# Kernel optimization log

Hardware: AMD Instinct MI355X
Metric: run time of the kernel (lower is better)

The kernel has to match this reference:

```python
import jax, jax.numpy as jnp
import numpy as np

L, D = 8192, 1024


def binary_operator_diag(q_i, q_j):
    # elementwise (diagonal) linear-recurrence combine: h_j = A_j * h_i + b_j
    A_i, b_i = q_i
    A_j, b_j = q_j
    return A_j * A_i, A_j * b_i + b_j


def setup_inputs() -> dict:
    key = jax.random.key(0)
    k_in, k_u, k_th, k_bre, k_bim = jax.random.split(key, 5)
    inputs = jax.random.normal(k_in, (L, D), dtype=jnp.float32)
    # stable LRU init: |lambda| = exp(-exp(nu)) = sqrt(u), u in (0.01, 0.99)
    u = jax.random.uniform(k_u, (D,), jnp.float32, 0.01, 0.99)
    nu = jnp.log(-0.5 * jnp.log(u))
    # phase stored in log-space (forward uses exp(theta))
    theta = jnp.log(jax.random.uniform(k_th, (D,), jnp.float32, 1e-3, 6.28))
    gamma_log = 0.5 * jnp.log(1.0 - u)  # = log(sqrt(1 - |lambda|^2))
    norm = np.float32(np.sqrt(2.0 * D))
    B_re = jax.random.normal(k_bre, (D, D), jnp.float32) / norm
    B_im = jax.random.normal(k_bim, (D, D), jnp.float32) / norm
    return {"inputs": inputs, "theta": theta, "nu": nu,
            "gamma_log": gamma_log, "B_re": B_re, "B_im": B_im}


def reference(inputs, theta, nu, gamma_log, B_re, B_im):
    # diagonal transition: lambda = exp(-exp(nu) + i*exp(theta)), shape [D]
    diag_lambda = jnp.exp(-jnp.exp(nu) + 1j * jnp.exp(theta))
    # normalized input matrix: (B_re + i B_im) * exp(gamma_log)[:, None]
    B_norm = (B_re + 1j * B_im) * jnp.exp(gamma_log)[:, None]  # [D, D] complex
    # Bu[t] = B_norm @ u_t  -> batched as one GEMM: [L, D] complex
    Bu = jnp.einsum('ld,kd->lk', inputs.astype(B_norm.dtype), B_norm)
    Lambda_elements = jnp.broadcast_to(diag_lambda[None, :], Bu.shape)
    # parallel associative scan over time (axis 0), elementwise over channels
    _, hidden_states = jax.lax.associative_scan(
        binary_operator_diag, (Lambda_elements, Bu))
    return hidden_states.real + inputs
```

## Files before the change

### kernel.cpp

```cpp
#include <hip/hip_runtime.h>
#include <cstdint>
#include <cstddef>

typedef float  f32x4   __attribute__((ext_vector_type(4)));
typedef short  bf16x8  __attribute__((ext_vector_type(8)));
typedef unsigned short u16x8 __attribute__((ext_vector_type(8)));

#define L_SEQ   8192
#define D_DIM   1024
#define N_COL   2048
#define N_PAIR  512
#define CHUNK_T 16
#define N_CHUNK 512

__device__ __forceinline__ unsigned short f2bf(float f) {
  unsigned int b = __float_as_uint(f);
  b += 0x7FFFu + ((b >> 16) & 1u);
  return (unsigned short)(b >> 16);
}
__device__ __forceinline__ float bf2f(unsigned short u) {
  return __uint_as_float((unsigned int)u << 16);
}
__device__ __forceinline__ void gload_lds16(const void* g, void* lds) {
  __builtin_amdgcn_global_load_lds(
      (const __attribute__((address_space(1))) void*)g,
      (__attribute__((address_space(3))) void*)lds, 16, 0, 0);
}
__device__ __forceinline__ float2 cmul(float2 a, float2 b) {
  return make_float2(a.x * b.x - a.y * b.y, a.x * b.y + a.y * b.x);
}
__device__ __forceinline__ float2 csqr(float2 a) {
  return make_float2(a.x * a.x - a.y * a.y, 2.f * a.x * a.y);
}
__device__ __forceinline__ void cfma2(const float4& lm, float2& h0, float2& h1,
                                      const float4& v) {
  float nr0 = fmaf(lm.x, h0.x, fmaf(-lm.y, h0.y, v.x));
  float ni0 = fmaf(lm.x, h0.y, fmaf(lm.y, h0.x, v.y));
  float nr1 = fmaf(lm.z, h1.x, fmaf(-lm.w, h1.y, v.z));
  float ni1 = fmaf(lm.z, h1.y, fmaf(lm.w, h1.x, v.w));
  h0.x = nr0; h0.y = ni0; h1.x = nr1; h1.y = ni1;
}

__global__ __launch_bounds__(256) void k_prep(
    const float* __restrict__ in, const float* __restrict__ Bre,
    const float* __restrict__ Bim, const float* __restrict__ gamma_log,
    const float* __restrict__ theta, const float* __restrict__ nu,
    unsigned short* __restrict__ A, unsigned short* __restrict__ W,
    float2* __restrict__ lam) {
  int b = blockIdx.x;
  if (b < 4096) {
    int i = b * 256 + threadIdx.x;
    const float4* p = (const float4*)in;
    float4 a = p[2 * i], c = p[2 * i + 1];
    u16x8 o;
    o[0] = f2bf(a.x); o[1] = f2bf(a.y); o[2] = f2bf(a.z); o[3] = f2bf(a.w);
    o[4] = f2bf(c.x); o[5] = f2bf(c.y); o[6] = f2bf(c.z); o[7] = f2bf(c.w);
    *(u16x8*)(A + (size_t)i * 8) = o;
  } else if (b < 5120) {
    int t = (b - 4096) * 256 + threadIdx.x;
    int row = t >> 7;
    int seg = t & 127;
    int k = row >> 1;
    const float* src = (row & 1) ? Bim : Bre;
    float g = expf(gamma_log[k]);
    const float4* p = (const float4*)(src + (size_t)k * D_DIM + seg * 8);
    float4 a = p[0], c = p[1];
    u16x8 o;
    o[0] = f2bf(a.x * g); o[1] = f2bf(a.y * g); o[2] = f2bf(a.z * g); o[3] = f2bf(a.w * g);
    o[4] = f2bf(c.x * g); o[5] = f2bf(c.y * g); o[6] = f2bf(c.z * g); o[7] = f2bf(c.w * g);
    *(u16x8*)(W + (size_t)row * D_DIM + seg * 8) = o;
  } else {
    int k = (b - 5120) * 256 + threadIdx.x;
    if (k < D_DIM) {
      float mod = expf(-expf(nu[k]));
      float ang = expf(theta[k]);
      lam[k] = make_float2(mod * cosf(ang), mod * sinf(ang));
    }
  }
}

__global__ __launch_bounds__(256, 2) void k_gemm(const unsigned short* __restrict__ A,
                                                 const unsigned short* __restrict__ W,
                                                 unsigned short* __restrict__ Bu16,
                                                 float2* __restrict__ agg2,
                                                 const float2* __restrict__ lam) {
  extern __shared__ char smem[];

  const int tid = threadIdx.x;
  const int l = tid & 63, w = tid >> 6;
  const int wm = w >> 1, wn = w & 1;

  int orig = blockIdx.x;
  int wgid = (orig & 7) * 64 + (orig >> 3);
  const int mt = wgid >> 4, nt = wgid & 15;
  const size_t m0 = (size_t)mt * 256, n0 = (size_t)nt * 128;

  const int sch = (tid & 3) ^ ((tid >> 3) & 3);
  const size_t soff = (size_t)(tid >> 2) * 2048 + (size_t)sch * 16;

#define STAGE(bb, TT) do {                                                          \
    const char* sa = (const char*)A + m0 * 2048 + (size_t)(TT) * 64;                \
    char* da = smem + (bb) * 16384;                                                 \
    gload_lds16(sa + soff,          da + tid * 16);                                 \
    gload_lds16(sa + 131072 + soff, da + 4096 + tid * 16);                          \
    gload_lds16(sa + 262144 + soff, da + 8192 + tid * 16);                          \
    gload_lds16(sa + 393216 + soff, da + 12288 + tid * 16);                         \
    const char* sb = (const char*)W + n0 * 2048 + (size_t)(TT) * 64;                \
    char* db = smem + 49152 + (bb) * 8192;                                          \
    gload_lds16(sb + soff,          db + tid * 16);                                 \
    gload_lds16(sb + 131072 + soff, db + 4096 + tid * 16);                          \
  } while (0)

  const int swk = (((l >> 4)) ^ ((l >> 1) & 3)) << 4;
  int aoff[8], boff[4];
#pragma unroll
  for (int fr = 0; fr < 8; ++fr)
    aoff[fr] = (wm * 128 + fr * 16 + (l & 15)) * 64 + swk;
#pragma unroll
  for (int fn = 0; fn < 4; ++fn)
    boff[fn] = (wn * 64 + fn * 16 + (l & 15)) * 64 + swk;

  f32x4 acc[8][4];
#pragma unroll
  for (int m = 0; m < 8; ++m)
#pragma unroll
    for (int n = 0; n < 4; ++n) acc[m][n] = (f32x4){0.f, 0.f, 0.f, 0.f};

#define VMCNT6 asm volatile("s_waitcnt vmcnt(6)" ::: "memory")
#define VMCNT0 asm volatile("s_waitcnt vmcnt(0)" ::: "memory")
#define BAR()  do { asm volatile("" ::: "memory"); __builtin_amdgcn_s_barrier(); \
                    asm volatile("" ::: "memory"); } while (0)

  STAGE(0, 0);
  STAGE(1, 1);
  VMCNT6;
  BAR();

  for (int kt = 0; kt < 32; ++kt) {
    const int rb = kt % 3;
    if (kt + 2 < 32) STAGE((kt + 2) % 3, kt + 2);
    const char* ab = smem + rb * 16384;
    const char* bb = smem + 49152 + rb * 8192;
    bf16x8 a_[8], b_[4];
#pragma unroll
    for (int fr = 0; fr < 8; ++fr) a_[fr] = *(const bf16x8*)(ab + aoff[fr]);
#pragma unroll
    for (int fn = 0; fn < 4; ++fn) b_[fn] = *(const bf16x8*)(bb + boff[fn]);
    __builtin_amdgcn_s_setprio(1);
#pragma unroll
    for (int fr = 0; fr < 8; ++fr)
#pragma unroll
      for (int fn = 0; fn < 4; ++fn)
        acc[fr][fn] = __builtin_amdgcn_mfma_f32_16x16x32_bf16(a_[fr], b_[fn],
                                                              acc[fr][fn], 0, 0, 0);
    __builtin_amdgcn_s_setprio(0);
    if (kt < 30) VMCNT6; else VMCNT0;
    BAR();
  }
#undef STAGE

#pragma unroll
  for (int fr = 0; fr < 8; ++fr)
#pragma unroll
    for (int fn = 0; fn < 4; ++fn) {
      int col = wn * 64 + fn * 16 + (l & 15);
#pragma unroll
      for (int j = 0; j < 4; ++j) {
        int row = wm * 128 + fr * 16 + (l >> 4) * 4 + j;
        int byte = row * 256 + ((col * 2) ^ ((row & 7) << 4));
        *(unsigned short*)(smem + byte) = f2bf(acc[fr][fn][j]);
      }
    }
  __syncthreads();

  {
    unsigned short* gbase = Bu16 + m0 * N_COL + n0;
#pragma unroll
    for (int pass = 0; pass < 16; ++pass) {
      int row = pass * 16 + (tid >> 4);
      int c = tid & 15;
      int byte = row * 256 + ((c * 16) ^ ((row & 7) << 4));
      f32x4 v = *(const f32x4*)(smem + byte);
      *(f32x4*)(gbase + (size_t)row * N_COL + c * 8) = v;
    }
  }

#pragma unroll
  for (int i = 0; i < 4; ++i) {
    int q = i * 256 + tid;
    int c = q >> 6, ch = q & 63;
    float2 lmv = lam[(n0 >> 1) + ch];
    unsigned int pr[16];
#pragma unroll
    for (int s = 0; s < 16; ++s) {
      int row = c * 16 + s;
      pr[s] = *(const unsigned int*)(smem + row * 256 + ((ch * 4) ^ ((row & 7) << 4)));
    }
    float2 h = {0.f, 0.f};
#pragma unroll
    for (int s = 0; s < 16; ++s) {
      float br = bf2f((unsigned short)(pr[s] & 0xFFFFu));
      float bi = bf2f((unsigned short)(pr[s] >> 16));
      float nr = fmaf(lmv.x, h.x, fmaf(-lmv.y, h.y, br));
      float ni = fmaf(lmv.x, h.y, fmaf(lmv.y, h.x, bi));
      h.x = nr; h.y = ni;
    }
    agg2[(size_t)(mt * 16 + c) * 1024 + (n0 >> 1) + ch] = h;
  }
}

__global__ __launch_bounds__(256) void k_scan2(const float4* __restrict__ agg4,
                                               const float4* __restrict__ lam4,
                                               float4* __restrict__ carry4) {
  int wave = blockIdx.x * 4 + (threadIdx.x >> 6);
  int lane = threadIdx.x & 63;
  int j = wave;
  float4 lm = lam4[j];
  float2 lT0 = {lm.x, lm.y}, lT1 = {lm.z, lm.w};
#pragma unroll
  for (int i = 0; i < 4; ++i) { lT0 = csqr(lT0); lT1 = csqr(lT1); }

  float4 a[8];
  float2 T0 = {0.f, 0.f}, T1 = {0.f, 0.f};
  float4 lTv = make_float4(lT0.x, lT0.y, lT1.x, lT1.y);
#pragma unroll
  for (int i = 0; i < 8; ++i) {
    a[i] = agg4[(size_t)(lane * 8 + i) * N_PAIR + j];
    cfma2(lTv, T0, T1, a[i]);
  }

  float2 M0 = lT0, M1 = lT1;
#pragma unroll
  for (int i = 0; i < 3; ++i) { M0 = csqr(M0); M1 = csqr(M1); }
  float2 S0 = T0, S1 = T1;
#pragma unroll
  for (int d = 1; d < 64; d <<= 1) {
    float2 u0, u1;
    u0.x = __shfl_up(S0.x, d); u0.y = __shfl_up(S0.y, d);
    u1.x = __shfl_up(S1.x, d); u1.y = __shfl_up(S1.y, d);
    if (lane >= d) {
      float2 m0 = cmul(M0, u0), m1 = cmul(M1, u1);
      S0.x += m0.x; S0.y += m0.y; S1.x += m1.x; S1.y += m1.y;
    }
    M0 = csqr(M0); M1 = csqr(M1);
  }
  float2 P0, P1;
  P0.x = __shfl_up(S0.x, 1); P0.y = __shfl_up(S0.y, 1);
  P1.x = __shfl_up(S1.x, 1); P1.y = __shfl_up(S1.y, 1);
  if (lane == 0) { P0 = make_float2(0.f, 0.f); P1 = make_float2(0.f, 0.f); }

#pragma unroll
  for (int i = 0; i < 8; ++i) {
    carry4[(size_t)(lane * 8 + i) * N_PAIR + j] = make_float4(P0.x, P0.y, P1.x, P1.y);
    cfma2(lTv, P0, P1, a[i]);
  }
}

__global__ __launch_bounds__(256) void k_scan3(const u16x8* __restrict__ Bu8,
                                               const float4* __restrict__ lam4,
                                               const float4* __restrict__ carry4,
                                               const ushort4* __restrict__ inA,
                                               float4* __restrict__ out4) {
  int t = blockIdx.x * 256 + threadIdx.x;
  int c = t >> 8, q = t & 255;
  float4 lm0 = lam4[2 * q], lm1 = lam4[2 * q + 1];
  float4 cv0 = carry4[(size_t)c * N_PAIR + 2 * q];
  float4 cv1 = carry4[(size_t)c * N_PAIR + 2 * q + 1];
  float2 h0 = {cv0.x, cv0.y}, h1 = {cv0.z, cv0.w};
  float2 h2 = {cv1.x, cv1.y}, h3 = {cv1.z, cv1.w};
#pragma unroll
  for (int s = 0; s < CHUNK_T; ++s) {
    size_t row = (size_t)c * CHUNK_T + s;
    u16x8 b = Bu8[row * 256 + q];
    float4 v0 = make_float4(bf2f(b[0]), bf2f(b[1]), bf2f(b[2]), bf2f(b[3]));
    float4 v1 = make_float4(bf2f(b[4]), bf2f(b[5]), bf2f(b[6]), bf2f(b[7]));
    cfma2(lm0, h0, h1, v0);
    cfma2(lm1, h2, h3, v1);
    ushort4 iv = inA[row * 256 + q];
    out4[row * 256 + q] = make_float4(h0.x + bf2f(iv.x), h1.x + bf2f(iv.y),
                                      h2.x + bf2f(iv.z), h3.x + bf2f(iv.w));
  }
}

extern "C" void kernel_launch(void* const* d_in, const int* in_sizes, int n_in,
                              void* d_out, int out_size, void* d_ws, size_t ws_size,
                              hipStream_t stream) {
  (void)in_sizes; (void)n_in; (void)out_size; (void)ws_size;
  const float* inputs    = (const float*)d_in[0];
  const float* theta     = (const float*)d_in[1];
  const float* nu        = (const float*)d_in[2];
  const float* gamma_log = (const float*)d_in[3];
  const float* Bre       = (const float*)d_in[4];
  const float* Bim       = (const float*)d_in[5];

  char* ws = (char*)d_ws;
  float2*         lam   = (float2*)ws;
  unsigned short* A     = (unsigned short*)(ws + (1 << 16));
  unsigned short* W     = (unsigned short*)(ws + (1 << 16) + (16u << 20));
  unsigned short* Bu16  = (unsigned short*)(ws + (1 << 16) + (20u << 20));
  float2*         agg   = (float2*)(ws + (1 << 16) + (52u << 20));
  float4*         carry = (float4*)(ws + (1 << 16) + (56u << 20));

  hipFuncSetAttribute((const void*)k_gemm,
                      hipFuncAttributeMaxDynamicSharedMemorySize, 73728);

  k_prep<<<5124, 256, 0, stream>>>(inputs, Bre, Bim, gamma_log, theta, nu, A, W, lam);
  k_gemm<<<512, 256, 73728, stream>>>(A, W, Bu16, agg, (const float2*)lam);
  k_scan2<<<N_PAIR / 4, 256, 0, stream>>>((const float4*)agg, (const float4*)lam, carry);
  k_scan3<<<(N_CHUNK * 256) / 256, 256, 0, stream>>>((const u16x8*)Bu16,
                                                     (const float4*)lam, carry,
                                                     (const ushort4*)A,
                                                     (float4*)d_out);
}
```

Before: 73.71 us.

## Load W fragments directly into registers and double-buffer A with K=64 steps

The GEMM no longer stages the weight tile through LDS. Each wave loads its B fragments straight from global memory into double-buffered registers. The A tile is now staged in 128-byte K slices with a two-buffer LDS ring instead of a three-buffer ring of 64-byte slices, which halves the number of barriers and iterations. The intent is to cut LDS traffic and synchronisation, but the loop now waits for all loads (vmcnt 0) every iteration, which weakens prefetch overlap and adds register pressure from the wA/wB arrays.

```diff
diff --git a/kernel.cpp b/kernel.cpp
--- a/kernel.cpp
+++ b/kernel.cpp
@@ -95,30 +95,34 @@
   const int mt = wgid >> 4, nt = wgid & 15;
   const size_t m0 = (size_t)mt * 256, n0 = (size_t)nt * 128;
 
-  const int sch = (tid & 3) ^ ((tid >> 3) & 3);
-  const size_t soff = (size_t)(tid >> 2) * 2048 + (size_t)sch * 16;
-
-#define STAGE(bb, TT) do {                                                          \
-    const char* sa = (const char*)A + m0 * 2048 + (size_t)(TT) * 64;                \
-    char* da = smem + (bb) * 16384;                                                 \
-    gload_lds16(sa + soff,          da + tid * 16);                                 \
-    gload_lds16(sa + 131072 + soff, da + 4096 + tid * 16);                          \
-    gload_lds16(sa + 262144 + soff, da + 8192 + tid * 16);                          \
-    gload_lds16(sa + 393216 + soff, da + 12288 + tid * 16);                         \
-    const char* sb = (const char*)W + n0 * 2048 + (size_t)(TT) * 64;                \
-    char* db = smem + 49152 + (bb) * 8192;                                          \
-    gload_lds16(sb + soff,          db + tid * 16);                                 \
-    gload_lds16(sb + 131072 + soff, db + 4096 + tid * 16);                          \
+  const int srow = tid >> 3, cs = tid & 7;
+  const int cA = cs ^ (srow & 7);
+
+#define STAGE_A(bb, TT) do {                                                        \
+    const char* s_ = (const char*)A + m0 * 2048 + (size_t)(TT) * 128;               \
+    char* d_ = smem + (bb) * 32768;                                                 \
+    _Pragma("unroll")                                                               \
+    for (int r_ = 0; r_ < 8; ++r_)                                                  \
+      gload_lds16(s_ + (size_t)(r_ * 32 + srow) * 2048 + cA * 16,                   \
+                  d_ + r_ * 4096 + tid * 16);                                       \
   } while (0)
 
-  const int swk = (((l >> 4)) ^ ((l >> 1) & 3)) << 4;
-  int aoff[8], boff[4];
+  const unsigned short* wbase = W + (n0 + wn * 64 + (l & 15)) * 1024 + (l >> 4) * 8;
+#define LOADW(dst, TT) do {                                                         \
+    _Pragma("unroll")                                                               \
+    for (int fn_ = 0; fn_ < 4; ++fn_)                                               \
+      _Pragma("unroll")                                                             \
+      for (int ks_ = 0; ks_ < 2; ++ks_)                                             \
+        dst[fn_ * 2 + ks_] = *(const bf16x8*)(wbase + (size_t)fn_ * 16384 +         \
+                                              (size_t)(TT) * 64 + ks_ * 32);        \
+  } while (0)
+
+  int aroff[8];
 #pragma unroll
   for (int fr = 0; fr < 8; ++fr)
-    aoff[fr] = (wm * 128 + fr * 16 + (l & 15)) * 64 + swk;
-#pragma unroll
-  for (int fn = 0; fn < 4; ++fn)
-    boff[fn] = (wn * 64 + fn * 16 + (l & 15)) * 64 + swk;
+    aroff[fr] = (wm * 128 + fr * 16 + (l & 15)) * 128;
+  const int swk0 = (((l >> 4)) ^ (l & 7)) << 4;
+  const int swk1 = ((4 + (l >> 4)) ^ (l & 7)) << 4;
 
   f32x4 acc[8][4];
 #pragma unroll
@@ -126,38 +130,55 @@
 #pragma unroll
     for (int n = 0; n < 4; ++n) acc[m][n] = (f32x4){0.f, 0.f, 0.f, 0.f};
 
-#define VMCNT6 asm volatile("s_waitcnt vmcnt(6)" ::: "memory")
+  bf16x8 wA[8], wB[8];
+
 #define VMCNT0 asm volatile("s_waitcnt vmcnt(0)" ::: "memory")
 #define BAR()  do { asm volatile("" ::: "memory"); __builtin_amdgcn_s_barrier(); \
                     asm volatile("" ::: "memory"); } while (0)
 
-  STAGE(0, 0);
-  STAGE(1, 1);
-  VMCNT6;
+  STAGE_A(0, 0);
+  LOADW(wA, 0);
+  VMCNT0;
   BAR();
 
-  for (int kt = 0; kt < 32; ++kt) {
-    const int rb = kt % 3;
-    if (kt + 2 < 32) STAGE((kt + 2) % 3, kt + 2);
-    const char* ab = smem + rb * 16384;
-    const char* bb = smem + 49152 + rb * 8192;
-    bf16x8 a_[8], b_[4];
-#pragma unroll
-    for (int fr = 0; fr < 8; ++fr) a_[fr] = *(const bf16x8*)(ab + aoff[fr]);
-#pragma unroll
-    for (int fn = 0; fn < 4; ++fn) b_[fn] = *(const bf16x8*)(bb + boff[fn]);
-    __builtin_amdgcn_s_setprio(1);
-#pragma unroll
-    for (int fr = 0; fr < 8; ++fr)
-#pragma unroll
-      for (int fn = 0; fn < 4; ++fn)
-        acc[fr][fn] = __builtin_amdgcn_mfma_f32_16x16x32_bf16(a_[fr], b_[fn],
-                                                              acc[fr][fn], 0, 0, 0);
-    __builtin_amdgcn_s_setprio(0);
-    if (kt < 30) VMCNT6; else VMCNT0;
-    BAR();
-  }
-#undef STAGE
+#define KT_BODY(KT, WCUR, WNXT) do {                                                \
+    const int bb_ = (KT) & 1;                                                       \
+    if ((KT) + 1 < 16) { STAGE_A(bb_ ^ 1, (KT) + 1); LOADW(WNXT, (KT) + 1); }       \
+    const char* ab_ = smem + bb_ * 32768;                                           \
+    bf16x8 a_[8];                                                                   \
+    _Pragma("unroll")                                                               \
+    for (int fr_ = 0; fr_ < 8; ++fr_)                                               \
+      a_[fr_] = *(const bf16x8*)(ab_ + aroff[fr_] + swk0);                          \
+    __builtin_amdgcn_s_setprio(1);                                                  \
+    _Pragma("unroll")                                                               \
+    for (int fr_ = 0; fr_ < 8; ++fr_)                                               \
+      _Pragma("unroll")                                                             \
+      for (int fn_ = 0; fn_ < 4; ++fn_)                                             \
+        acc[fr_][fn_] = __builtin_amdgcn_mfma_f32_16x16x32_bf16(                    \
+            a_[fr_], WCUR[fn_ * 2], acc[fr_][fn_], 0, 0, 0);                        \
+    __builtin_amdgcn_s_setprio(0);                                                  \
+    _Pragma("unroll")                                                               \
+    for (int fr_ = 0; fr_ < 8; ++fr_)                                               \
+      a_[fr_] = *(const bf16x8*)(ab_ + aroff[fr_] + swk1);                          \
+    __builtin_amdgcn_s_setprio(1);                                                  \
+    _Pragma("unroll")                                                               \
+    for (int fr_ = 0; fr_ < 8; ++fr_)                                               \
+      _Pragma("unroll")                                                             \
+      for (int fn_ = 0; fn_ < 4; ++fn_)                                             \
+        acc[fr_][fn_] = __builtin_amdgcn_mfma_f32_16x16x32_bf16(                    \
+            a_[fr_], WCUR[fn_ * 2 + 1], acc[fr_][fn_], 0, 0, 0);                    \
+    __builtin_amdgcn_s_setprio(0);                                                  \
+    VMCNT0;                                                                         \
+    BAR();                                                                          \
+  } while (0)
+
+  for (int kt2 = 0; kt2 < 16; kt2 += 2) {
+    KT_BODY(kt2, wA, wB);
+    KT_BODY(kt2 + 1, wB, wA);
+  }
+#undef KT_BODY
+#undef STAGE_A
+#undef LOADW
 
 #pragma unroll
   for (int fr = 0; fr < 8; ++fr)
@@ -302,10 +323,10 @@
   float4*         carry = (float4*)(ws + (1 << 16) + (56u << 20));
 
   hipFuncSetAttribute((const void*)k_gemm,
-                      hipFuncAttributeMaxDynamicSharedMemorySize, 73728);
+                      hipFuncAttributeMaxDynamicSharedMemorySize, 65536);
 
   k_prep<<<5124, 256, 0, stream>>>(inputs, Bre, Bim, gamma_log, theta, nu, A, W, lam);
-  k_gemm<<<512, 256, 73728, stream>>>(A, W, Bu16, agg, (const float2*)lam);
+  k_gemm<<<512, 256, 65536, stream>>>(A, W, Bu16, agg, (const float2*)lam);
   k_scan2<<<N_PAIR / 4, 256, 0, stream>>>((const float4*)agg, (const float4*)lam, carry);
   k_scan3<<<(N_CHUNK * 256) / 256, 256, 0, stream>>>((const u16x8*)Bu16,
                                                      (const float4*)lam, carry,
```

After: 114.0 us. 1.55x slower.
